# Optimization experiments

Hardware: AMD Instinct MI355X
Metric: run time of the kernel (lower is better)

## Reference

```python
import jax, jax.numpy as jnp
import numpy as np

B, T, C, H = 8, 2048, 1024, 128  # batch, seq, embed_dim, head_size

def setup_inputs() -> dict:
    key = jax.random.key(0)
    kx, kk, kq, kv = jax.random.split(key, 4)
    s = 1.0 / np.sqrt(C)  # ~nn.Linear init scale
    return {
        "x": jax.random.normal(kx, (B, T, C), dtype=jnp.float32),
        "Wk": jax.random.normal(kk, (H, C), dtype=jnp.float32) * s,
        "Wq": jax.random.normal(kq, (H, C), dtype=jnp.float32) * s,
        "Wv": jax.random.normal(kv, (H, C), dtype=jnp.float32) * s,
    }

def reference(x, Wk, Wq, Wv):
    b, t, c = x.shape
    # Faithful to source: q uses the KEY projection (bug in original); Wq is unused.
    k = jnp.einsum('btc,hc->bth', x, Wk)   # [B,T,H]
    q = jnp.einsum('btc,hc->bth', x, Wk)   # [B,T,H]  (self.key used for q)
    v = jnp.einsum('btc,hc->bth', x, Wv)   # [B,T,H]
    score = jnp.einsum('bqh,bkh->bqk', q, k) * (c ** -0.5)  # scale by C, per source
    causal = jnp.tril(jnp.ones((t, t), dtype=bool))
    score = jnp.where(causal, score, -jnp.inf)
    attn = jax.nn.softmax(score, axis=-1)   # [B,T,T]
    out = jnp.einsum('bqk,bkh->bqh', attn, v)  # [B,T,H]
    return out
```

## Files before the change

kernel.cpp:

```cpp
#include <hip/hip_runtime.h>
#include <hip/hip_bf16.h>

#define BATCH 8
#define SEQ   2048
#define EMB   1024
#define HD    128

typedef __attribute__((ext_vector_type(8))) short bf16x8;
typedef __attribute__((ext_vector_type(4))) float f32x4;

__device__ __forceinline__ short f2bf(float f) {
    union { float f; unsigned u; } v; v.f = f;
    unsigned r = v.u + 0x7fffu + ((v.u >> 16) & 1u);
    return (short)(r >> 16);
}

__device__ __forceinline__ void glds16(const short* g, short* l) {
    __builtin_amdgcn_global_load_lds(
        (const __attribute__((address_space(1))) unsigned int*)g,
        (__attribute__((address_space(3))) unsigned int*)l, 16, 0, 0);
}


__global__ void prep_w(const float* __restrict__ Wk, const float* __restrict__ Wv,
                       short* __restrict__ Wimg) {
    int g  = blockIdx.x * 256 + threadIdx.x;
    int q  = g & 3;
    int l  = (g >> 2) & 15;
    int f  = (g >> 6) & 7;
    int kk = (g >> 9) & 1;
    int kc = (g >> 10) & 15;
    int nh = (g >> 14) & 1;
    const float* src = (nh ? Wv : Wk) + (size_t)(f * 16 + l) * EMB + kc * 64 + kk * 32 + q * 8;
    float4 f0 = *(const float4*)src;
    float4 f1 = *(const float4*)(src + 4);
    bf16x8 v;
    v[0]=f2bf(f0.x); v[1]=f2bf(f0.y); v[2]=f2bf(f0.z); v[3]=f2bf(f0.w);
    v[4]=f2bf(f1.x); v[5]=f2bf(f1.y); v[6]=f2bf(f1.z); v[7]=f2bf(f1.w);
    *(bf16x8*)&Wimg[(size_t)g * 8] = v;
}

__global__ __launch_bounds__(512, 2)
void proj_kernel(const float* __restrict__ x, const short* __restrict__ Wimg,
                 short* __restrict__ Kimg,
                 short* __restrict__ Vimg)
{
    __shared__ __align__(16) union {
        short A[2][64][72];
        short ep[16384];
    } sm;

    const int tid  = threadIdx.x;
    const int wave = tid >> 6;
    const int lane = tid & 63;
    const int quad = lane >> 4;
    const int l16  = lane & 15;
    const int nh   = wave >> 2;
    const int fb   = (wave & 3) * 2;
    const int mt   = blockIdx.x;
    const int row0 = mt * 64;

    const int srow = tid >> 3, sseg = tid & 7;
    const float* xsrc = x + (size_t)(row0 + srow) * EMB + sseg * 8;
    const short* wsrc = Wimg + (size_t)nh * 131072;

    f32x4 acc[4][2];
#pragma unroll
    for (int a = 0; a < 4; ++a)
#pragma unroll
        for (int c = 0; c < 2; ++c) acc[a][c] = f32x4{0.f, 0.f, 0.f, 0.f};

    {
        float4 a0 = *(const float4*)xsrc;
        float4 a1 = *(const float4*)(xsrc + 4);
        bf16x8 v;
        v[0]=f2bf(a0.x); v[1]=f2bf(a0.y); v[2]=f2bf(a0.z); v[3]=f2bf(a0.w);
        v[4]=f2bf(a1.x); v[5]=f2bf(a1.y); v[6]=f2bf(a1.z); v[7]=f2bf(a1.w);
        *(bf16x8*)&sm.A[0][srow][sseg * 8] = v;
    }
    __syncthreads();

    for (int kc = 0; kc < 16; ++kc) {
        const int cur = kc & 1;
        float4 a0, a1;
        if (kc < 15) {
            const float* nx = xsrc + (kc + 1) * 64;
            a0 = *(const float4*)nx;
            a1 = *(const float4*)(nx + 4);
        }
        const short* wc = wsrc + (size_t)kc * 8192;
        bf16x8 bfr[2][2];
#pragma unroll
        for (int kk = 0; kk < 2; ++kk)
#pragma unroll
            for (int f2 = 0; f2 < 2; ++f2)
                bfr[kk][f2] = *(const bf16x8*)&wc[(((kk * 8 + fb + f2) * 16 + l16) * 4 + quad) * 8];

#pragma unroll
        for (int kk = 0; kk < 2; ++kk)
#pragma unroll
            for (int mf = 0; mf < 4; ++mf) {
                bf16x8 af = *(const bf16x8*)&sm.A[cur][mf * 16 + l16][kk * 32 + quad * 8];
#pragma unroll
                for (int f2 = 0; f2 < 2; ++f2)
                    acc[mf][f2] = __builtin_amdgcn_mfma_f32_16x16x32_bf16(af, bfr[kk][f2], acc[mf][f2], 0, 0, 0);
            }

        if (kc < 15) {
            bf16x8 v;
            v[0]=f2bf(a0.x); v[1]=f2bf(a0.y); v[2]=f2bf(a0.z); v[3]=f2bf(a0.w);
            v[4]=f2bf(a1.x); v[5]=f2bf(a1.y); v[6]=f2bf(a1.z); v[7]=f2bf(a1.w);
            *(bf16x8*)&sm.A[cur ^ 1][srow][sseg * 8] = v;
        }
        __syncthreads();
    }

#pragma unroll
    for (int mf = 0; mf < 4; ++mf)
#pragma unroll
        for (int f2 = 0; f2 < 2; ++f2)
#pragma unroll
            for (int r = 0; r < 4; ++r) {
                const int row = mf * 16 + quad * 4 + r;
                const int h   = (fb + f2) * 16 + l16;
                int idx;
                if (nh == 0)
                    idx = ((((h >> 5) * 4 + (row >> 4)) * 16 + (row & 15)) * 4 + ((h >> 3) & 3)) * 8 + (h & 7);
                else
                    idx = 8192 + ((((row >> 5) * 8 + (h >> 4)) * 16 + (h & 15)) * 4 + ((row >> 3) & 3)) * 8 + (row & 7);
                sm.ep[idx] = f2bf(acc[mf][f2][r]);
            }
    __syncthreads();

    {
#pragma unroll
        for (int i = 0; i < 4; ++i) {
            const int g = i * 512 + tid;
            short* dst = (g < 1024) ? (Kimg + (size_t)mt * 8192 + g * 8)
                                    : (Vimg + (size_t)mt * 8192 + (g - 1024) * 8);
            *(bf16x8*)dst = *(const bf16x8*)&sm.ep[g * 8];
        }
    }
}

#define LOG2E 1.4426950408889634f

__global__ __launch_bounds__(512, 2)
void attn_kernel(const short* __restrict__ Kimg,
                 const short* __restrict__ Vimg,
                 float* __restrict__ out)
{
    __shared__ __align__(16) short kbuf[2][8192];
    __shared__ __align__(16) short vbuf[8192];
    __shared__ __align__(16) short ps[4][1024];
    __shared__ float lsum[8][16];

    const int tid  = threadIdx.x;
    const int wave = tid >> 6;
    const int lane = tid & 63;
    const int quad = lane >> 4;
    const int l16  = lane & 15;

    const int b    = blockIdx.x & 7;
    const int G    = 31 - (blockIdx.x >> 3);
    const int qsel = wave >> 1;
    const int p    = wave & 1;
    const int qt   = 4 * G + qsel;
    const int n    = G + 1;

    const short* Kb = Kimg + (size_t)b * 32 * 8192;
    const short* Vb = Vimg + (size_t)b * 32 * 8192;

    bf16x8 qf[4];
    {
        const short* qi = Kb + (size_t)G * 8192;
#pragma unroll
        for (int kc = 0; kc < 4; ++kc)
            qf[kc] = *(const bf16x8*)&qi[(((kc * 4 + qsel) * 16 + l16) * 4 + quad) * 8];
    }

    f32x4 O[4];
#pragma unroll
    for (int f = 0; f < 4; ++f) O[f] = f32x4{0.f, 0.f, 0.f, 0.f};
    float lp[4] = {0.f, 0.f, 0.f, 0.f};

    const float coef = LOG2E * 0.03125f;
    short* psq = ps[qsel];

    {
        const short* sk = Kb + wave * 1024 + lane * 8;
#pragma unroll
        for (int i = 0; i < 2; ++i)
            glds16(sk + i * 512, &kbuf[0][wave * 1024 + i * 512]);
    }

    int cur = 0;
    for (int jt = 0; jt < n; ++jt) {
        asm volatile("s_waitcnt vmcnt(0)" ::: "memory");
        __builtin_amdgcn_s_barrier();

        {
            const short* sv = Vb + (size_t)jt * 8192 + wave * 1024 + lane * 8;
#pragma unroll
            for (int i = 0; i < 2; ++i)
                glds16(sv + i * 512, &vbuf[wave * 1024 + i * 512]);
        }
        const bool more = (jt + 1 < n);
        if (more) {
            const short* sk = Kb + (size_t)(jt + 1) * 8192 + wave * 1024 + lane * 8;
#pragma unroll
            for (int i = 0; i < 2; ++i)
                glds16(sk + i * 512, &kbuf[cur ^ 1][wave * 1024 + i * 512]);
        }

        const short* kt = kbuf[cur];
        f32x4 S[2];
        S[0] = f32x4{0.f, 0.f, 0.f, 0.f};
        S[1] = f32x4{0.f, 0.f, 0.f, 0.f};
#pragma unroll
        for (int kc = 0; kc < 4; ++kc)
#pragma unroll
            for (int j2 = 0; j2 < 2; ++j2) {
                bf16x8 kf = *(const bf16x8*)&kt[((kc * 4 + p * 2 + j2) * 64 + l16 * 4 + quad) * 8];
                S[j2] = __builtin_amdgcn_mfma_f32_16x16x32_bf16(qf[kc], kf, S[j2], 0, 0, 0);
            }

        const bool diag = (jt == n - 1);
#pragma unroll
        for (int j2 = 0; j2 < 2; ++j2) {
            const int js = p * 2 + j2;
            const int jj = jt * 64 + js * 16 + l16;
            const int cb = js * 2 + (l16 >> 3);
            const int e  = l16 & 7;
#pragma unroll
            for (int r = 0; r < 4; ++r) {
                float vv = S[j2][r] * coef;
                if (diag && (jj > qt * 16 + quad * 4 + r)) vv = -INFINITY;
                float pe = exp2f(vv);
                lp[r] += pe;
                const int i8 = quad * 4 + r;
                psq[(i8 * 8 + (cb ^ (i8 & 7))) * 8 + e] = f2bf(pe);
            }
        }

        if (more) asm volatile("s_waitcnt vmcnt(2) lgkmcnt(0)" ::: "memory");
        else      asm volatile("s_waitcnt vmcnt(0) lgkmcnt(0)" ::: "memory");
        __builtin_amdgcn_s_barrier();

#pragma unroll
        for (int jc = 0; jc < 2; ++jc) {
            const int pblk = l16 * 8 + ((jc * 4 + quad) ^ (l16 & 7));
            bf16x8 pa = *(const bf16x8*)&psq[pblk * 8];
#pragma unroll
            for (int fo = 0; fo < 4; ++fo) {
                bf16x8 vf = *(const bf16x8*)&vbuf[((jc * 8 + p * 4 + fo) * 64 + l16 * 4 + quad) * 8];
                O[fo] = __builtin_amdgcn_mfma_f32_16x16x32_bf16(pa, vf, O[fo], 0, 0, 0);
            }
        }
        cur ^= 1;
    }

#pragma unroll
    for (int r = 0; r < 4; ++r) {
        float s = lp[r];
        s += __shfl_xor(s, 1);
        s += __shfl_xor(s, 2);
        s += __shfl_xor(s, 4);
        s += __shfl_xor(s, 8);
        lp[r] = s;
    }
    if (l16 == 0) {
#pragma unroll
        for (int r = 0; r < 4; ++r) lsum[wave][quad * 4 + r] = lp[r];
    }
    __syncthreads();

#pragma unroll
    for (int r = 0; r < 4; ++r) {
        const int row16 = quad * 4 + r;
        const float L   = lsum[qsel * 2][row16] + lsum[qsel * 2 + 1][row16];
        const float inv = 1.f / L;
        const int row   = qt * 16 + row16;
        float* dst = out + (size_t)(b * SEQ + row) * HD + p * 64 + l16;
#pragma unroll
        for (int fo = 0; fo < 4; ++fo)
            dst[fo * 16] = O[fo][r] * inv;
    }
}

extern "C" void kernel_launch(void* const* d_in, const int* in_sizes, int n_in,
                              void* d_out, int out_size, void* d_ws, size_t ws_size,
                              hipStream_t stream) {
    const float* x  = (const float*)d_in[0];
    const float* Wk = (const float*)d_in[1];
    const float* Wv = (const float*)d_in[3];
    float* out = (float*)d_out;

    short* Wimg = (short*)d_ws;
    short* Kimg = Wimg + (size_t)262144;
    short* Vimg = Kimg + (size_t)BATCH * 32 * 8192;

    prep_w<<<128, 256, 0, stream>>>(Wk, Wv, Wimg);
    proj_kernel<<<256, 512, 0, stream>>>(x, Wimg, Kimg, Vimg);
    attn_kernel<<<256, 512, 0, stream>>>(Kimg, Vimg, out);
}
```

Baseline: 153.0 us.

## Balance causal attention work by splitting long query tiles across blocks

Rebalances the causal workload across blocks. Query groups with index 17 and above have their key range split in two: one block processes keys 0..16, and a second block that also handles a short group processes the remainder. The two partial outputs and row sums go to a workspace buffer, and whichever block finishes second, tracked by an atomic counter, merges them. This evens out per-block iteration counts so the grid tail is shorter. The cost is extra global traffic for the partials, extra fences, syncs and an atomic, plus a counter reset added to prep_w.

```diff
diff --git a/kernel.cpp b/kernel.cpp
--- a/kernel.cpp
+++ b/kernel.cpp
@@ -23,7 +23,8 @@
 
 
 __global__ void prep_w(const float* __restrict__ Wk, const float* __restrict__ Wv,
-                       short* __restrict__ Wimg) {
+                       short* __restrict__ Wimg, int* __restrict__ cnt) {
+    if (blockIdx.x == 0 && threadIdx.x < 256) cnt[threadIdx.x] = 0;
     int g  = blockIdx.x * 256 + threadIdx.x;
     int q  = g & 3;
     int l  = (g >> 2) & 15;
@@ -148,12 +149,15 @@
 __global__ __launch_bounds__(512, 2)
 void attn_kernel(const short* __restrict__ Kimg,
                  const short* __restrict__ Vimg,
-                 float* __restrict__ out)
+                 float* __restrict__ out,
+                 float* __restrict__ pbase,
+                 int* __restrict__ cnt)
 {
     __shared__ __align__(16) short kbuf[2][8192];
     __shared__ __align__(16) short vbuf[8192];
     __shared__ __align__(16) short ps[4][1024];
     __shared__ float lsum[8][16];
+    __shared__ int sflag;
 
     const int tid  = threadIdx.x;
     const int wave = tid >> 6;
@@ -162,129 +166,179 @@
     const int l16  = lane & 15;
 
     const int b    = blockIdx.x & 7;
-    const int G    = 31 - (blockIdx.x >> 3);
+    const int idx  = blockIdx.x >> 3;
     const int qsel = wave >> 1;
     const int p    = wave & 1;
-    const int qt   = 4 * G + qsel;
-    const int n    = G + 1;
 
     const short* Kb = Kimg + (size_t)b * 32 * 8192;
     const short* Vb = Vimg + (size_t)b * 32 * 8192;
-
-    bf16x8 qf[4];
-    {
-        const short* qi = Kb + (size_t)G * 8192;
-#pragma unroll
-        for (int kc = 0; kc < 4; ++kc)
-            qf[kc] = *(const bf16x8*)&qi[(((kc * 4 + qsel) * 16 + l16) * 4 + quad) * 8];
-    }
-
-    f32x4 O[4];
-#pragma unroll
-    for (int f = 0; f < 4; ++f) O[f] = f32x4{0.f, 0.f, 0.f, 0.f};
-    float lp[4] = {0.f, 0.f, 0.f, 0.f};
-
     const float coef = LOG2E * 0.03125f;
     short* psq = ps[qsel];
 
-    {
-        const short* sk = Kb + wave * 1024 + lane * 8;
-#pragma unroll
-        for (int i = 0; i < 2; ++i)
-            glds16(sk + i * 512, &kbuf[0][wave * 1024 + i * 512]);
-    }
-
-    int cur = 0;
-    for (int jt = 0; jt < n; ++jt) {
-        asm volatile("s_waitcnt vmcnt(0)" ::: "memory");
-        __builtin_amdgcn_s_barrier();
-
+    auto run_phase = [&](int Gp, int j0, int j1, int mode) {
+        const int qt = 4 * Gp + qsel;
+
+        bf16x8 qf[4];
         {
-            const short* sv = Vb + (size_t)jt * 8192 + wave * 1024 + lane * 8;
+            const short* qi = Kb + (size_t)Gp * 8192;
+#pragma unroll
+            for (int kc = 0; kc < 4; ++kc)
+                qf[kc] = *(const bf16x8*)&qi[(((kc * 4 + qsel) * 16 + l16) * 4 + quad) * 8];
+        }
+
+        f32x4 O[4];
+#pragma unroll
+        for (int f = 0; f < 4; ++f) O[f] = f32x4{0.f, 0.f, 0.f, 0.f};
+        float lp[4] = {0.f, 0.f, 0.f, 0.f};
+
+        {
+            const short* sk = Kb + (size_t)j0 * 8192 + wave * 1024 + lane * 8;
 #pragma unroll
             for (int i = 0; i < 2; ++i)
-                glds16(sv + i * 512, &vbuf[wave * 1024 + i * 512]);
-        }
-        const bool more = (jt + 1 < n);
-        if (more) {
-            const short* sk = Kb + (size_t)(jt + 1) * 8192 + wave * 1024 + lane * 8;
-#pragma unroll
-            for (int i = 0; i < 2; ++i)
-                glds16(sk + i * 512, &kbuf[cur ^ 1][wave * 1024 + i * 512]);
-        }
-
-        const short* kt = kbuf[cur];
-        f32x4 S[2];
-        S[0] = f32x4{0.f, 0.f, 0.f, 0.f};
-        S[1] = f32x4{0.f, 0.f, 0.f, 0.f};
-#pragma unroll
-        for (int kc = 0; kc < 4; ++kc)
+                glds16(sk + i * 512, &kbuf[0][wave * 1024 + i * 512]);
+        }
+
+        int cur = 0;
+        for (int jt = j0; jt < j1; ++jt) {
+            asm volatile("s_waitcnt vmcnt(0)" ::: "memory");
+            __builtin_amdgcn_s_barrier();
+
+            {
+                const short* sv = Vb + (size_t)jt * 8192 + wave * 1024 + lane * 8;
+#pragma unroll
+                for (int i = 0; i < 2; ++i)
+                    glds16(sv + i * 512, &vbuf[wave * 1024 + i * 512]);
+            }
+            const bool more = (jt + 1 < j1);
+            if (more) {
+                const short* sk = Kb + (size_t)(jt + 1) * 8192 + wave * 1024 + lane * 8;
+#pragma unroll
+                for (int i = 0; i < 2; ++i)
+                    glds16(sk + i * 512, &kbuf[cur ^ 1][wave * 1024 + i * 512]);
+            }
+
+            const short* kt = kbuf[cur];
+            f32x4 S[2];
+            S[0] = f32x4{0.f, 0.f, 0.f, 0.f};
+            S[1] = f32x4{0.f, 0.f, 0.f, 0.f};
+#pragma unroll
+            for (int kc = 0; kc < 4; ++kc)
+#pragma unroll
+                for (int j2 = 0; j2 < 2; ++j2) {
+                    bf16x8 kf = *(const bf16x8*)&kt[((kc * 4 + p * 2 + j2) * 64 + l16 * 4 + quad) * 8];
+                    S[j2] = __builtin_amdgcn_mfma_f32_16x16x32_bf16(qf[kc], kf, S[j2], 0, 0, 0);
+                }
+
+            const bool diag = (jt == Gp);
 #pragma unroll
             for (int j2 = 0; j2 < 2; ++j2) {
-                bf16x8 kf = *(const bf16x8*)&kt[((kc * 4 + p * 2 + j2) * 64 + l16 * 4 + quad) * 8];
-                S[j2] = __builtin_amdgcn_mfma_f32_16x16x32_bf16(qf[kc], kf, S[j2], 0, 0, 0);
-            }
-
-        const bool diag = (jt == n - 1);
-#pragma unroll
-        for (int j2 = 0; j2 < 2; ++j2) {
-            const int js = p * 2 + j2;
-            const int jj = jt * 64 + js * 16 + l16;
-            const int cb = js * 2 + (l16 >> 3);
-            const int e  = l16 & 7;
+                const int js = p * 2 + j2;
+                const int jj = jt * 64 + js * 16 + l16;
+                const int cb = js * 2 + (l16 >> 3);
+                const int e  = l16 & 7;
+#pragma unroll
+                for (int r = 0; r < 4; ++r) {
+                    float vv = S[j2][r] * coef;
+                    if (diag && (jj > qt * 16 + quad * 4 + r)) vv = -INFINITY;
+                    float pe = exp2f(vv);
+                    lp[r] += pe;
+                    const int i8 = quad * 4 + r;
+                    psq[(i8 * 8 + (cb ^ (i8 & 7))) * 8 + e] = f2bf(pe);
+                }
+            }
+
+            if (more) asm volatile("s_waitcnt vmcnt(2) lgkmcnt(0)" ::: "memory");
+            else      asm volatile("s_waitcnt vmcnt(0) lgkmcnt(0)" ::: "memory");
+            __builtin_amdgcn_s_barrier();
+
+#pragma unroll
+            for (int jc = 0; jc < 2; ++jc) {
+                const int pblk = l16 * 8 + ((jc * 4 + quad) ^ (l16 & 7));
+                bf16x8 pa = *(const bf16x8*)&psq[pblk * 8];
+#pragma unroll
+                for (int fo = 0; fo < 4; ++fo) {
+                    bf16x8 vf = *(const bf16x8*)&vbuf[((jc * 8 + p * 4 + fo) * 64 + l16 * 4 + quad) * 8];
+                    O[fo] = __builtin_amdgcn_mfma_f32_16x16x32_bf16(pa, vf, O[fo], 0, 0, 0);
+                }
+            }
+            cur ^= 1;
+        }
+
+#pragma unroll
+        for (int r = 0; r < 4; ++r) {
+            float s = lp[r];
+            s += __shfl_xor(s, 1);
+            s += __shfl_xor(s, 2);
+            s += __shfl_xor(s, 4);
+            s += __shfl_xor(s, 8);
+            lp[r] = s;
+        }
+        __syncthreads();
+        if (l16 == 0) {
+#pragma unroll
+            for (int r = 0; r < 4; ++r) lsum[wave][quad * 4 + r] = lp[r];
+        }
+        __syncthreads();
+
+        float Lp[4];
+#pragma unroll
+        for (int r = 0; r < 4; ++r)
+            Lp[r] = lsum[qsel * 2][quad * 4 + r] + lsum[qsel * 2 + 1][quad * 4 + r];
+
+        if (mode == 0) {
 #pragma unroll
             for (int r = 0; r < 4; ++r) {
-                float vv = S[j2][r] * coef;
-                if (diag && (jj > qt * 16 + quad * 4 + r)) vv = -INFINITY;
-                float pe = exp2f(vv);
-                lp[r] += pe;
-                const int i8 = quad * 4 + r;
-                psq[(i8 * 8 + (cb ^ (i8 & 7))) * 8 + e] = f2bf(pe);
-            }
-        }
-
-        if (more) asm volatile("s_waitcnt vmcnt(2) lgkmcnt(0)" ::: "memory");
-        else      asm volatile("s_waitcnt vmcnt(0) lgkmcnt(0)" ::: "memory");
-        __builtin_amdgcn_s_barrier();
-
-#pragma unroll
-        for (int jc = 0; jc < 2; ++jc) {
-            const int pblk = l16 * 8 + ((jc * 4 + quad) ^ (l16 & 7));
-            bf16x8 pa = *(const bf16x8*)&psq[pblk * 8];
-#pragma unroll
-            for (int fo = 0; fo < 4; ++fo) {
-                bf16x8 vf = *(const bf16x8*)&vbuf[((jc * 8 + p * 4 + fo) * 64 + l16 * 4 + quad) * 8];
-                O[fo] = __builtin_amdgcn_mfma_f32_16x16x32_bf16(pa, vf, O[fo], 0, 0, 0);
-            }
-        }
-        cur ^= 1;
-    }
-
-#pragma unroll
-    for (int r = 0; r < 4; ++r) {
-        float s = lp[r];
-        s += __shfl_xor(s, 1);
-        s += __shfl_xor(s, 2);
-        s += __shfl_xor(s, 4);
-        s += __shfl_xor(s, 8);
-        lp[r] = s;
-    }
-    if (l16 == 0) {
-#pragma unroll
-        for (int r = 0; r < 4; ++r) lsum[wave][quad * 4 + r] = lp[r];
-    }
-    __syncthreads();
-
-#pragma unroll
-    for (int r = 0; r < 4; ++r) {
-        const int row16 = quad * 4 + r;
-        const float L   = lsum[qsel * 2][row16] + lsum[qsel * 2 + 1][row16];
-        const float inv = 1.f / L;
-        const int row   = qt * 16 + row16;
-        float* dst = out + (size_t)(b * SEQ + row) * HD + p * 64 + l16;
-#pragma unroll
-        for (int fo = 0; fo < 4; ++fo)
-            dst[fo * 16] = O[fo][r] * inv;
+                const int row16 = quad * 4 + r;
+                const float inv = 1.f / Lp[r];
+                const int row   = qt * 16 + row16;
+                float* dst = out + (size_t)(b * SEQ + row) * HD + p * 64 + l16;
+#pragma unroll
+                for (int fo = 0; fo < 4; ++fo)
+                    dst[fo * 16] = O[fo][r] * inv;
+            }
+        } else {
+            float* slot = pbase + (size_t)(b * 15 + (Gp - 17)) * 16896;
+            float* my   = slot + (mode == 1 ? 0 : 8448);
+            float* oth  = slot + (mode == 1 ? 8448 : 0);
+#pragma unroll
+            for (int fo = 0; fo < 4; ++fo)
+#pragma unroll
+                for (int r = 0; r < 4; ++r)
+                    my[(fo * 4 + r) * 512 + tid] = O[fo][r];
+            if (p == 0 && l16 == 0) {
+#pragma unroll
+                for (int r = 0; r < 4; ++r)
+                    my[8192 + qsel * 16 + quad * 4 + r] = Lp[r];
+            }
+            __threadfence();
+            __syncthreads();
+            if (tid == 0) sflag = atomicAdd(&cnt[b * 32 + Gp], 1);
+            __syncthreads();
+            if (sflag == 1) {
+                __threadfence();
+#pragma unroll
+                for (int r = 0; r < 4; ++r) {
+                    const int row16 = quad * 4 + r;
+                    const float L   = Lp[r] + oth[8192 + qsel * 16 + row16];
+                    const float inv = 1.f / L;
+                    const int row   = qt * 16 + row16;
+                    float* dst = out + (size_t)(b * SEQ + row) * HD + p * 64 + l16;
+#pragma unroll
+                    for (int fo = 0; fo < 4; ++fo)
+                        dst[fo * 16] = (O[fo][r] + oth[(fo * 4 + r) * 512 + tid]) * inv;
+                }
+            }
+        }
+    };
+
+    if (idx < 16) {
+        const int G = 16 + idx;
+        run_phase(G, 0, 17, (G == 16) ? 0 : 1);
+    } else {
+        const int Gl = idx - 16;
+        const int Gh = 47 - idx;
+        run_phase(Gl, 0, Gl + 1, 0);
+        if (Gh >= 17) run_phase(Gh, 17, Gh + 1, 2);
     }
 }
 
@@ -299,8 +353,10 @@
     short* Wimg = (short*)d_ws;
     short* Kimg = Wimg + (size_t)262144;
     short* Vimg = Kimg + (size_t)BATCH * 32 * 8192;
-
-    prep_w<<<128, 256, 0, stream>>>(Wk, Wv, Wimg);
+    float* pbase = (float*)(Vimg + (size_t)BATCH * 32 * 8192);
+    int*   cnt   = (int*)(pbase + (size_t)120 * 16896);
+
+    prep_w<<<128, 256, 0, stream>>>(Wk, Wv, Wimg, cnt);
     proj_kernel<<<256, 512, 0, stream>>>(x, Wimg, Kimg, Vimg);
-    attn_kernel<<<256, 512, 0, stream>>>(Kimg, Vimg, out);
-}
+    attn_kernel<<<256, 512, 0, stream>>>(Kimg, Vimg, out, pbase, cnt);
+}
```

Measured after the change: 207.8 us. 35.8% more time.
